# Kernel tuning notes

Hardware: AMD Instinct MI355X
Metric: run time of the kernel (lower is better)

## Reference

```python
import jax, jax.numpy as jnp
import numpy as np

H = 16
D_K = 64
WINDOW = 4  # hardcoded window_size in the original attention()


def setup_inputs() -> dict:
    key = jax.random.key(0)
    ks = jax.random.split(key, 11)
    B, S, D = 4, 2048, 1024
    s = 1.0 / np.sqrt(D)
    return {
        "query": jax.random.normal(ks[0], (B, S, D), jnp.float32),
        "key": jax.random.normal(ks[1], (B, S, D), jnp.float32),
        "value": jax.random.normal(ks[2], (B, S, D), jnp.float32),
        # torch Linear weights stored transposed ([in,out]) so y = x @ W + b
        "Wq": jax.random.normal(ks[3], (D, D), jnp.float32) * s,
        "bq": jnp.zeros((D,), jnp.float32),
        "Wk": jax.random.normal(ks[4], (D, D), jnp.float32) * s,
        "bk": jnp.zeros((D,), jnp.float32),
        "Wv": jax.random.normal(ks[5], (D, D), jnp.float32) * s,
        "bv": jnp.zeros((D,), jnp.float32),
        "Wo": jax.random.normal(ks[6], (D, D), jnp.float32) * s,
        "bo": jnp.zeros((D,), jnp.float32),
    }


def _split_heads(x, B, S):
    # [B,S,D] -> [B,H,S,d_k]
    return x.reshape(B, S, H, D_K).transpose(0, 2, 1, 3)


def reference(query, key, value, Wq, bq, Wk, bk, Wv, bv, Wo, bo):
    B, S, D = query.shape
    q = _split_heads(query @ Wq + bq, B, S)
    k = _split_heads(key @ Wk + bk, B, S)
    v = _split_heads(value @ Wv + bv, B, S)

    scores = jnp.einsum("bhqd,bhkd->bhqk", q, k) / np.sqrt(D_K)
    # banded local-window enhancement: double scores where |i-j| <= WINDOW
    i = jnp.arange(S)[:, None]
    j = jnp.arange(S)[None, :]
    band = (jnp.abs(i - j) <= WINDOW).astype(scores.dtype)  # [S,S]
    enhanced = scores * (1.0 + band)  # scores + scores*local_mask

    p_attn = jax.nn.softmax(enhanced, axis=-1)  # dropout = identity (eval)
    out = jnp.einsum("bhqk,bhkd->bhqd", p_attn, v)
    out = out.transpose(0, 2, 1, 3).reshape(B, S, D)
    return out @ Wo + bo
```

## Files before the change

### kernel.cpp

```cpp
#include <hip/hip_runtime.h>
#include <hip/hip_bf16.h>

typedef __attribute__((ext_vector_type(8))) short short8;
typedef __attribute__((ext_vector_type(4))) float f32x4;
typedef __attribute__((ext_vector_type(16))) float f32x16;

#define DEVINL static __device__ __forceinline__

DEVINL unsigned short f2b(float f) {
  __hip_bfloat16 h = __float2bfloat16(f);
  return __builtin_bit_cast(unsigned short, h);
}

DEVINL float fexp2(float x) {
#if __has_builtin(__builtin_amdgcn_exp2f)
  return __builtin_amdgcn_exp2f(x);
#else
  float r; asm("v_exp_f32 %0, %1\n\ts_nop 0" : "=v"(r) : "v"(x)); return r;
#endif
}

DEVINL unsigned cvt_pk_bf16(float a, float b) {
  unsigned r;
  asm("v_cvt_pk_bf16_f32 %0, %1, %2" : "=v"(r) : "v"(a), "v"(b));
  return r;
}

DEVINL void pl32swap(unsigned& a, unsigned& b) {
  asm volatile("v_permlane32_swap_b32 %0, %1" : "+v"(a), "+v"(b));
}

DEVINL void gload_lds16(const unsigned short* gsrc, unsigned short* ldst) {
  __builtin_amdgcn_global_load_lds(
      (const __attribute__((address_space(1))) unsigned int*)gsrc,
      (__attribute__((address_space(3))) unsigned int*)ldst,
      16, 0, 0);
}

__global__ __launch_bounds__(256)
void cvt_act_kernel(const float* __restrict__ in, unsigned short* __restrict__ out) {
  const long i = ((long)blockIdx.x * 256 + threadIdx.x) * 8;
  const float4 a = *reinterpret_cast<const float4*>(in + i);
  const float4 b = *reinterpret_cast<const float4*>(in + i + 4);
  uint4 o;
  o.x = f2b(a.x) | ((unsigned)f2b(a.y) << 16);
  o.y = f2b(a.z) | ((unsigned)f2b(a.w) << 16);
  o.z = f2b(b.x) | ((unsigned)f2b(b.y) << 16);
  o.w = f2b(b.z) | ((unsigned)f2b(b.w) << 16);
  *reinterpret_cast<uint4*>(out + i) = o;
}

__global__ __launch_bounds__(256)
void cvt_w_kernel(const float* __restrict__ W0, const float* __restrict__ W1,
                  const float* __restrict__ W2, const float* __restrict__ W3,
                  unsigned short* __restrict__ WtAll) {
  __shared__ __align__(16) unsigned short t[64][72];
  const float* W = blockIdx.z == 0 ? W0 : blockIdx.z == 1 ? W1 : blockIdx.z == 2 ? W2 : W3;
  unsigned short* out = WtAll + (size_t)blockIdx.z * (1024 * 1024);
  const int tid = threadIdx.x;
  const int k0 = blockIdx.y * 64, n0 = blockIdx.x * 64;
  const int r = tid >> 2;
  const int c = (tid & 3) * 16;
  #pragma unroll
  for (int u = 0; u < 4; ++u) {
    float4 v = *reinterpret_cast<const float4*>(W + (long)(k0 + r) * 1024 + n0 + c + u * 4);
    t[c + u*4 + 0][r] = f2b(v.x);
    t[c + u*4 + 1][r] = f2b(v.y);
    t[c + u*4 + 2][r] = f2b(v.z);
    t[c + u*4 + 3][r] = f2b(v.w);
  }
  __syncthreads();
  #pragma unroll
  for (int u = 0; u < 2; ++u)
    *reinterpret_cast<uint4*>(out + (long)(n0 + r) * 1024 + k0 + c + u * 8) =
        *reinterpret_cast<const uint4*>(&t[r][c + u * 8]);
}

template<int MODE>
__global__ __launch_bounds__(256)
void gemm_bf16_kernel(const unsigned short* __restrict__ A,
                      const unsigned short* __restrict__ Wt,
                      const float* __restrict__ bias, void* __restrict__ outp,
                      int M, int N, int K, float oscale)
{
  __shared__ __align__(16) unsigned short Asm[128 * 64];
  __shared__ __align__(16) unsigned short Bsm[128 * 64];

  const int tid = threadIdx.x;
  const int lane = tid & 63;
  const int wid = tid >> 6;
  const int l15 = lane & 15;
  const int lg  = lane >> 4;

  const int nwg = gridDim.x;
  const int cpx = nwg >> 3;
  const int wg  = blockIdx.x;
  const int swz = (wg & 7) * cpx + (wg >> 3);
  const int nbx = N >> 7;
  const long bm = (long)(swz / nbx) * 128;
  const long bn = (long)(swz % nbx) * 128;
  const int wm = (wid >> 1) * 64;
  const int wn = (wid & 1) * 64;

  const unsigned short* gA[4];
  const unsigned short* gB[4];
  unsigned ldsU[4];
  #pragma unroll
  for (int j = 0; j < 4; ++j) {
    const int t0 = j * 256 + wid * 64;
    const int task = t0 + lane;
    gA[j] = A  + (bm + (task >> 3)) * (long)K + (task & 7) * 8;
    gB[j] = Wt + (bn + (task >> 3)) * (long)K + (task & 7) * 8;
    ldsU[j] = (unsigned)t0 * 8;
  }

  f32x4 acc[4][4] = {};

  for (int kt = 0; kt < K; kt += 64) {
    #pragma unroll
    for (int j = 0; j < 4; ++j) {
      gload_lds16(gA[j] + kt, Asm + ldsU[j]);
      gload_lds16(gB[j] + kt, Bsm + ldsU[j]);
    }
    __syncthreads();

    short8 af[2][4], bf[2][4];
    #pragma unroll
    for (int m = 0; m < 4; ++m) {
      const unsigned short* pa = Asm + (wm + m * 16 + l15) * 64 + lg * 8;
      af[0][m] = *reinterpret_cast<const short8*>(pa);
      af[1][m] = *reinterpret_cast<const short8*>(pa + 32);
    }
    #pragma unroll
    for (int n = 0; n < 4; ++n) {
      const unsigned short* pb = Bsm + (wn + n * 16 + l15) * 64 + lg * 8;
      bf[0][n] = *reinterpret_cast<const short8*>(pb);
      bf[1][n] = *reinterpret_cast<const short8*>(pb + 32);
    }
    #pragma unroll
    for (int kk = 0; kk < 2; ++kk)
      #pragma unroll
      for (int m = 0; m < 4; ++m)
        #pragma unroll
        for (int n = 0; n < 4; ++n)
          acc[m][n] = __builtin_amdgcn_mfma_f32_16x16x32_bf16(af[kk][m], bf[kk][n], acc[m][n], 0, 0, 0);
    __syncthreads();
  }

  float bv[4];
  #pragma unroll
  for (int n = 0; n < 4; ++n) bv[n] = bias[bn + wn + n * 16 + l15];

  if (MODE == 1) {
    float* out = (float*)outp;
    #pragma unroll
    for (int m = 0; m < 4; ++m)
      #pragma unroll
      for (int r = 0; r < 4; ++r) {
        long row = bm + wm + m * 16 + lg * 4 + r;
        #pragma unroll
        for (int n = 0; n < 4; ++n)
          out[row * N + bn + wn + n * 16 + l15] = (acc[m][n][r] + bv[n]) * oscale;
      }
  } else if (MODE == 0) {
    unsigned short* out = (unsigned short*)outp;
    #pragma unroll
    for (int m = 0; m < 4; ++m)
      #pragma unroll
      for (int r = 0; r < 4; ++r) {
        long row = bm + wm + m * 16 + lg * 4 + r;
        long b = row >> 11, s = row & 2047;
        #pragma unroll
        for (int n = 0; n < 4; ++n) {
          long col = bn + wn + n * 16 + l15;
          long h = col >> 6, dk = col & 63;
          out[((((b << 4) + h) << 11) + s) * 64 + dk] = f2b((acc[m][n][r] + bv[n]) * oscale);
        }
      }
  } else {
    unsigned short* out = (unsigned short*)outp;
    #pragma unroll
    for (int m = 0; m < 4; ++m) {
      long row0 = bm + wm + m * 16 + lg * 4;
      long b = row0 >> 11, s0 = row0 & 2047;
      #pragma unroll
      for (int n = 0; n < 4; ++n) {
        long col = bn + wn + n * 16 + l15;
        long h = col >> 6, dk = col & 63;
        ushort4 hv;
        hv.x = f2b(acc[m][n][0] + bv[n]);
        hv.y = f2b(acc[m][n][1] + bv[n]);
        hv.z = f2b(acc[m][n][2] + bv[n]);
        hv.w = f2b(acc[m][n][3] + bv[n]);
        *reinterpret_cast<ushort4*>(&out[((((b << 4) + h) << 6) + dk) * 2048 + s0]) = hv;
      }
    }
  }
}

__global__ __launch_bounds__(512)
void attn_kernel(const unsigned short* __restrict__ Q,
                 const unsigned short* __restrict__ Kh,
                 const unsigned short* __restrict__ Vth,
                 unsigned short* __restrict__ Obf)
{
  __shared__ __align__(16) char lds[16384];

  const int tid = threadIdx.x;
  const int lane = tid & 63;
  const int w = tid >> 6;
  const int l31 = lane & 31;
  const int hi  = lane >> 5;
  const int r7  = l31 & 7;
  const int bh = blockIdx.x;
  const int wq = blockIdx.y * 256 + w * 32;
  const long base  = (long)bh * 2048 * 64;
  const long vbase = (long)bh * 64 * 2048;

  short8 aq[4];
  {
    const unsigned short* qp = Q + base + (long)(wq + l31) * 64 + hi * 8;
    #pragma unroll
    for (int sl = 0; sl < 4; ++sl)
      aq[sl] = *reinterpret_cast<const short8*>(qp + sl * 16);
  }

  const int srow = tid >> 3;
  const int sdst = (srow * 128 + (tid & 7) * 16) ^ ((srow & 7) << 4);
  const unsigned short* kgp = Kh + base + srow * 64 + (tid & 7) * 8;
  const unsigned short* vgp = Vth + vbase + (long)srow * 2048 + (tid & 7) * 8;

  uint4 kreg = *reinterpret_cast<const uint4*>(kgp);
  uint4 vreg = *reinterpret_cast<const uint4*>(vgp);

  f32x16 oacc0 = {}, oacc1 = {};
  float mrun = -1e30f, lrun = 0.f;

  for (int kvt = 0; kvt < 2048; kvt += 64) {
    __syncthreads();
    *reinterpret_cast<uint4*>(lds + sdst) = kreg;
    *reinterpret_cast<uint4*>(lds + 8192 + sdst) = vreg;
    __syncthreads();
    if (kvt + 64 < 2048) {
      kreg = *reinterpret_cast<const uint4*>(kgp + (kvt + 64) * 64);
      vreg = *reinterpret_cast<const uint4*>(vgp + (kvt + 64));
    }

    short8 ak[4][2], av[4][2];
    #pragma unroll
    for (int n = 0; n < 4; ++n) {
      #pragma unroll
      for (int half = 0; half < 2; ++half) {
        const int row = half * 32 + l31;
        const int slot = (((n * 2 + hi) ^ r7) << 4);
        ak[n][half] = *reinterpret_cast<const short8*>(lds + row * 128 + slot);
        av[n][half] = *reinterpret_cast<const short8*>(lds + 8192 + row * 128 + slot);
      }
    }

    f32x16 st0 = {}, st1 = {};
    #pragma unroll
    for (int sl = 0; sl < 4; ++sl) {
      st0 = __builtin_amdgcn_mfma_f32_32x32x16_bf16(ak[sl][0], aq[sl], st0, 0, 0, 0);
      st1 = __builtin_amdgcn_mfma_f32_32x32x16_bf16(ak[sl][1], aq[sl], st1, 0, 0, 0);
    }

    if ((kvt <= wq + 35) && (kvt + 67 >= wq)) {
      const int db0 = wq + l31 - kvt - 4 * hi;
      #pragma unroll
      for (int r = 0; r < 16; ++r) {
        const int rr = (r & 3) + 8 * (r >> 2);
        int d0 = db0 - rr;
        int d1 = db0 - 32 - rr;
        if (d0 >= -4 && d0 <= 4) st0[r] *= 2.f;
        if (d1 >= -4 && d1 <= 4) st1[r] *= 2.f;
      }
    }

    float tm[16];
    #pragma unroll
    for (int r = 0; r < 16; ++r) tm[r] = fmaxf(st0[r], st1[r]);
    #pragma unroll
    for (int s2 = 8; s2 >= 1; s2 >>= 1)
      #pragma unroll
      for (int r = 0; r < s2; ++r) tm[r] = fmaxf(tm[r], tm[r + s2]);
    float pmax = fmaxf(tm[0], __shfl_xor(tm[0], 32));

    if (pmax > mrun + 8.f) {
      float corr = fexp2(mrun - pmax);
      lrun *= corr;
      #pragma unroll
      for (int r = 0; r < 16; ++r) { oacc0[r] *= corr; oacc1[r] *= corr; }
      mrun = pmax;
    }

    #pragma unroll
    for (int r = 0; r < 16; ++r) {
      st0[r] = fexp2(st0[r] - mrun);
      st1[r] = fexp2(st1[r] - mrun);
    }
    float ts[16];
    #pragma unroll
    for (int r = 0; r < 16; ++r) ts[r] = st0[r] + st1[r];
    #pragma unroll
    for (int s2 = 8; s2 >= 1; s2 >>= 1)
      #pragma unroll
      for (int r = 0; r < s2; ++r) ts[r] += ts[r + s2];
    lrun += ts[0] + __shfl_xor(ts[0], 32);

    unsigned own0[8], own1[8];
    #pragma unroll
    for (int p = 0; p < 8; ++p) {
      own0[p] = cvt_pk_bf16(st0[2 * p], st0[2 * p + 1]);
      own1[p] = cvt_pk_bf16(st1[2 * p], st1[2 * p + 1]);
    }

    #pragma unroll
    for (int sl = 0; sl < 4; ++sl) {
      unsigned* ow = (sl < 2) ? own0 : own1;
      const int c4 = (sl & 1) * 4;
      pl32swap(ow[c4 + 0], ow[c4 + 2]);
      pl32swap(ow[c4 + 1], ow[c4 + 3]);
      uint4 pwv;
      pwv.x = ow[c4 + 0]; pwv.y = ow[c4 + 1]; pwv.z = ow[c4 + 2]; pwv.w = ow[c4 + 3];
      short8 pf = __builtin_bit_cast(short8, pwv);
      oacc0 = __builtin_amdgcn_mfma_f32_32x32x16_bf16(av[sl][0], pf, oacc0, 0, 0, 0);
      oacc1 = __builtin_amdgcn_mfma_f32_32x32x16_bf16(av[sl][1], pf, oacc1, 0, 0, 0);
    }
  }

  const int b = bh >> 4, h = bh & 15;
  const float inv = 1.f / lrun;
  unsigned short* op = Obf + ((long)(b * 2048 + wq + l31) << 10) + h * 64 + 4 * hi;
  #pragma unroll
  for (int g = 0; g < 4; ++g) {
    ushort4 u0, u1;
    u0.x = f2b(oacc0[4 * g + 0] * inv); u0.y = f2b(oacc0[4 * g + 1] * inv);
    u0.z = f2b(oacc0[4 * g + 2] * inv); u0.w = f2b(oacc0[4 * g + 3] * inv);
    u1.x = f2b(oacc1[4 * g + 0] * inv); u1.y = f2b(oacc1[4 * g + 1] * inv);
    u1.z = f2b(oacc1[4 * g + 2] * inv); u1.w = f2b(oacc1[4 * g + 3] * inv);
    *reinterpret_cast<ushort4*>(op + 8 * g) = u0;
    *reinterpret_cast<ushort4*>(op + 8 * g + 32) = u1;
  }
}

extern "C" void kernel_launch(void* const* d_in, const int* in_sizes, int n_in,
                              void* d_out, int out_size, void* d_ws, size_t ws_size,
                              hipStream_t stream)
{
  const float* query = (const float*)d_in[0];
  const float* key_  = (const float*)d_in[1];
  const float* value = (const float*)d_in[2];
  const float* Wq = (const float*)d_in[3];
  const float* bq = (const float*)d_in[4];
  const float* Wk = (const float*)d_in[5];
  const float* bk = (const float*)d_in[6];
  const float* Wv = (const float*)d_in[7];
  const float* bv = (const float*)d_in[8];
  const float* Wo = (const float*)d_in[9];
  const float* bo = (const float*)d_in[10];

  char* ws = (char*)d_ws;
  unsigned short* actbf = (unsigned short*)(ws);
  unsigned short* qh = (unsigned short*)(ws + ((size_t)16 << 20));
  unsigned short* kh = (unsigned short*)(ws + ((size_t)32 << 20));
  unsigned short* vt = (unsigned short*)(ws + ((size_t)48 << 20));
  unsigned short* WT = (unsigned short*)(ws + ((size_t)64 << 20));
  unsigned short* aout = actbf;

  const int Mrows = 4 * 2048, D = 1024;
  const float QSCALE = 0.125f * 1.44269504088896340736f;

  cvt_w_kernel<<<dim3(16, 16, 4), 256, 0, stream>>>(Wq, Wk, Wv, Wo, WT);

  cvt_act_kernel<<<4096, 256, 0, stream>>>(query, actbf);
  gemm_bf16_kernel<0><<<512, 256, 0, stream>>>(actbf, WT, bq, qh, Mrows, D, D, QSCALE);

  cvt_act_kernel<<<4096, 256, 0, stream>>>(key_, actbf);
  gemm_bf16_kernel<0><<<512, 256, 0, stream>>>(actbf, WT + (1 << 20), bk, kh, Mrows, D, D, 1.f);

  cvt_act_kernel<<<4096, 256, 0, stream>>>(value, actbf);
  gemm_bf16_kernel<2><<<512, 256, 0, stream>>>(actbf, WT + (2 << 20), bv, vt, Mrows, D, D, 1.f);

  attn_kernel<<<dim3(64, 8), 512, 0, stream>>>(qh, kh, vt, aout);

  gemm_bf16_kernel<1><<<512, 256, 0, stream>>>(aout, WT + (3 << 20), bo, (float*)d_out, Mrows, D, D, 1.f);
}
```

Baseline: 248.8 us.

## Fuse fp32-to-bf16 activation conversion into batched QKV projection GEMM

Removes the three separate activation conversion kernels. A single QKV GEMM launch with grid z=3 loads fp32 activations straight into registers, converts them to bf16 and stores them into LDS, with the next tile's A loads issued during the MFMA compute. This avoids writing and rereading a bf16 copy of each activation and cuts the number of launches. The trade-off is that A is now staged through registers instead of the direct global-to-LDS path, and fp32 reads each K tile twice as many bytes, which may lower GEMM efficiency.

New measurement: 224.9 us. -9.6%, faster.

```diff
diff --git a/kernel.cpp b/kernel.cpp
--- a/kernel.cpp
+++ b/kernel.cpp
@@ -35,19 +35,6 @@
       (const __attribute__((address_space(1))) unsigned int*)gsrc,
       (__attribute__((address_space(3))) unsigned int*)ldst,
       16, 0, 0);
-}
-
-__global__ __launch_bounds__(256)
-void cvt_act_kernel(const float* __restrict__ in, unsigned short* __restrict__ out) {
-  const long i = ((long)blockIdx.x * 256 + threadIdx.x) * 8;
-  const float4 a = *reinterpret_cast<const float4*>(in + i);
-  const float4 b = *reinterpret_cast<const float4*>(in + i + 4);
-  uint4 o;
-  o.x = f2b(a.x) | ((unsigned)f2b(a.y) << 16);
-  o.y = f2b(a.z) | ((unsigned)f2b(a.w) << 16);
-  o.z = f2b(b.x) | ((unsigned)f2b(b.y) << 16);
-  o.w = f2b(b.z) | ((unsigned)f2b(b.w) << 16);
-  *reinterpret_cast<uint4*>(out + i) = o;
 }
 
 __global__ __launch_bounds__(256)
@@ -76,15 +63,24 @@
         *reinterpret_cast<const uint4*>(&t[r][c + u * 8]);
 }
 
-template<int MODE>
 __global__ __launch_bounds__(256)
-void gemm_bf16_kernel(const unsigned short* __restrict__ A,
-                      const unsigned short* __restrict__ Wt,
-                      const float* __restrict__ bias, void* __restrict__ outp,
-                      int M, int N, int K, float oscale)
+void qkv_gemm_kernel(const float* __restrict__ Aq, const float* __restrict__ Ak,
+                     const float* __restrict__ Av,
+                     const unsigned short* __restrict__ WTall,
+                     const float* __restrict__ bq, const float* __restrict__ bk,
+                     const float* __restrict__ bv,
+                     unsigned short* __restrict__ qh, unsigned short* __restrict__ kh,
+                     unsigned short* __restrict__ vt, float qscale)
 {
+  constexpr int N = 1024, K = 1024;
   __shared__ __align__(16) unsigned short Asm[128 * 64];
   __shared__ __align__(16) unsigned short Bsm[128 * 64];
+
+  const int z = blockIdx.z;
+  const float* A = z == 0 ? Aq : z == 1 ? Ak : Av;
+  const unsigned short* Wt = WTall + ((size_t)z << 20);
+  const float* bias = z == 0 ? bq : z == 1 ? bk : bv;
+  const float oscale = z == 0 ? qscale : 1.f;
 
   const int tid = threadIdx.x;
   const int lane = tid & 63;
@@ -102,27 +98,50 @@
   const int wm = (wid >> 1) * 64;
   const int wn = (wid & 1) * 64;
 
-  const unsigned short* gA[4];
+  const float* gAf[4];
   const unsigned short* gB[4];
   unsigned ldsU[4];
+  int ldsE[4];
   #pragma unroll
   for (int j = 0; j < 4; ++j) {
     const int t0 = j * 256 + wid * 64;
     const int task = t0 + lane;
-    gA[j] = A  + (bm + (task >> 3)) * (long)K + (task & 7) * 8;
-    gB[j] = Wt + (bn + (task >> 3)) * (long)K + (task & 7) * 8;
+    gAf[j] = A  + (bm + (task >> 3)) * (long)K + (task & 7) * 8;
+    gB[j]  = Wt + (bn + (task >> 3)) * (long)K + (task & 7) * 8;
     ldsU[j] = (unsigned)t0 * 8;
+    ldsE[j] = task * 8;
   }
 
   f32x4 acc[4][4] = {};
 
+  float4 ra[4][2];
+  #pragma unroll
+  for (int j = 0; j < 4; ++j) {
+    ra[j][0] = *reinterpret_cast<const float4*>(gAf[j]);
+    ra[j][1] = *reinterpret_cast<const float4*>(gAf[j] + 4);
+  }
+
   for (int kt = 0; kt < K; kt += 64) {
     #pragma unroll
+    for (int j = 0; j < 4; ++j)
+      gload_lds16(gB[j] + kt, Bsm + ldsU[j]);
+    #pragma unroll
     for (int j = 0; j < 4; ++j) {
-      gload_lds16(gA[j] + kt, Asm + ldsU[j]);
-      gload_lds16(gB[j] + kt, Bsm + ldsU[j]);
-    }
-    __syncthreads();
+      uint4 o;
+      o.x = cvt_pk_bf16(ra[j][0].x, ra[j][0].y);
+      o.y = cvt_pk_bf16(ra[j][0].z, ra[j][0].w);
+      o.z = cvt_pk_bf16(ra[j][1].x, ra[j][1].y);
+      o.w = cvt_pk_bf16(ra[j][1].z, ra[j][1].w);
+      *reinterpret_cast<uint4*>(Asm + ldsE[j]) = o;
+    }
+    __syncthreads();
+    if (kt + 64 < K) {
+      #pragma unroll
+      for (int j = 0; j < 4; ++j) {
+        ra[j][0] = *reinterpret_cast<const float4*>(gAf[j] + kt + 64);
+        ra[j][1] = *reinterpret_cast<const float4*>(gAf[j] + kt + 68);
+      }
+    }
 
     short8 af[2][4], bf[2][4];
     #pragma unroll
@@ -147,23 +166,12 @@
     __syncthreads();
   }
 
-  float bv[4];
-  #pragma unroll
-  for (int n = 0; n < 4; ++n) bv[n] = bias[bn + wn + n * 16 + l15];
-
-  if (MODE == 1) {
-    float* out = (float*)outp;
-    #pragma unroll
-    for (int m = 0; m < 4; ++m)
-      #pragma unroll
-      for (int r = 0; r < 4; ++r) {
-        long row = bm + wm + m * 16 + lg * 4 + r;
-        #pragma unroll
-        for (int n = 0; n < 4; ++n)
-          out[row * N + bn + wn + n * 16 + l15] = (acc[m][n][r] + bv[n]) * oscale;
-      }
-  } else if (MODE == 0) {
-    unsigned short* out = (unsigned short*)outp;
+  float bvv[4];
+  #pragma unroll
+  for (int n = 0; n < 4; ++n) bvv[n] = bias[bn + wn + n * 16 + l15];
+
+  if (z < 2) {
+    unsigned short* out = z == 0 ? qh : kh;
     #pragma unroll
     for (int m = 0; m < 4; ++m)
       #pragma unroll
@@ -174,11 +182,11 @@
         for (int n = 0; n < 4; ++n) {
           long col = bn + wn + n * 16 + l15;
           long h = col >> 6, dk = col & 63;
-          out[((((b << 4) + h) << 11) + s) * 64 + dk] = f2b((acc[m][n][r] + bv[n]) * oscale);
+          out[((((b << 4) + h) << 11) + s) * 64 + dk] = f2b((acc[m][n][r] + bvv[n]) * oscale);
         }
       }
   } else {
-    unsigned short* out = (unsigned short*)outp;
+    unsigned short* out = vt;
     #pragma unroll
     for (int m = 0; m < 4; ++m) {
       long row0 = bm + wm + m * 16 + lg * 4;
@@ -188,14 +196,99 @@
         long col = bn + wn + n * 16 + l15;
         long h = col >> 6, dk = col & 63;
         ushort4 hv;
-        hv.x = f2b(acc[m][n][0] + bv[n]);
-        hv.y = f2b(acc[m][n][1] + bv[n]);
-        hv.z = f2b(acc[m][n][2] + bv[n]);
-        hv.w = f2b(acc[m][n][3] + bv[n]);
+        hv.x = f2b(acc[m][n][0] + bvv[n]);
+        hv.y = f2b(acc[m][n][1] + bvv[n]);
+        hv.z = f2b(acc[m][n][2] + bvv[n]);
+        hv.w = f2b(acc[m][n][3] + bvv[n]);
         *reinterpret_cast<ushort4*>(&out[((((b << 4) + h) << 6) + dk) * 2048 + s0]) = hv;
       }
     }
   }
+}
+
+__global__ __launch_bounds__(256)
+void gemm_out_kernel(const unsigned short* __restrict__ A,
+                     const unsigned short* __restrict__ Wt,
+                     const float* __restrict__ bias, float* __restrict__ out,
+                     int M, int N, int K)
+{
+  __shared__ __align__(16) unsigned short Asm[128 * 64];
+  __shared__ __align__(16) unsigned short Bsm[128 * 64];
+
+  const int tid = threadIdx.x;
+  const int lane = tid & 63;
+  const int wid = tid >> 6;
+  const int l15 = lane & 15;
+  const int lg  = lane >> 4;
+
+  const int nwg = gridDim.x;
+  const int cpx = nwg >> 3;
+  const int wg  = blockIdx.x;
+  const int swz = (wg & 7) * cpx + (wg >> 3);
+  const int nbx = N >> 7;
+  const long bm = (long)(swz / nbx) * 128;
+  const long bn = (long)(swz % nbx) * 128;
+  const int wm = (wid >> 1) * 64;
+  const int wn = (wid & 1) * 64;
+
+  const unsigned short* gA[4];
+  const unsigned short* gB[4];
+  unsigned ldsU[4];
+  #pragma unroll
+  for (int j = 0; j < 4; ++j) {
+    const int t0 = j * 256 + wid * 64;
+    const int task = t0 + lane;
+    gA[j] = A  + (bm + (task >> 3)) * (long)K + (task & 7) * 8;
+    gB[j] = Wt + (bn + (task >> 3)) * (long)K + (task & 7) * 8;
+    ldsU[j] = (unsigned)t0 * 8;
+  }
+
+  f32x4 acc[4][4] = {};
+
+  for (int kt = 0; kt < K; kt += 64) {
+    #pragma unroll
+    for (int j = 0; j < 4; ++j) {
+      gload_lds16(gA[j] + kt, Asm + ldsU[j]);
+      gload_lds16(gB[j] + kt, Bsm + ldsU[j]);
+    }
+    __syncthreads();
+
+    short8 af[2][4], bf[2][4];
+    #pragma unroll
+    for (int m = 0; m < 4; ++m) {
+      const unsigned short* pa = Asm + (wm + m * 16 + l15) * 64 + lg * 8;
+      af[0][m] = *reinterpret_cast<const short8*>(pa);
+      af[1][m] = *reinterpret_cast<const short8*>(pa + 32);
+    }
+    #pragma unroll
+    for (int n = 0; n < 4; ++n) {
+      const unsigned short* pb = Bsm + (wn + n * 16 + l15) * 64 + lg * 8;
+      bf[0][n] = *reinterpret_cast<const short8*>(pb);
+      bf[1][n] = *reinterpret_cast<const short8*>(pb + 32);
+    }
+    #pragma unroll
+    for (int kk = 0; kk < 2; ++kk)
+      #pragma unroll
+      for (int m = 0; m < 4; ++m)
+        #pragma unroll
+        for (int n = 0; n < 4; ++n)
+          acc[m][n] = __builtin_amdgcn_mfma_f32_16x16x32_bf16(af[kk][m], bf[kk][n], acc[m][n], 0, 0, 0);
+    __syncthreads();
+  }
+
+  float bvv[4];
+  #pragma unroll
+  for (int n = 0; n < 4; ++n) bvv[n] = bias[bn + wn + n * 16 + l15];
+
+  #pragma unroll
+  for (int m = 0; m < 4; ++m)
+    #pragma unroll
+    for (int r = 0; r < 4; ++r) {
+      long row = bm + wm + m * 16 + lg * 4 + r;
+      #pragma unroll
+      for (int n = 0; n < 4; ++n)
+        out[row * N + bn + wn + n * 16 + l15] = acc[m][n][r] + bvv[n];
+    }
 }
 
 __global__ __launch_bounds__(512)
@@ -361,28 +454,22 @@
   const float* bo = (const float*)d_in[10];
 
   char* ws = (char*)d_ws;
-  unsigned short* actbf = (unsigned short*)(ws);
+  unsigned short* aout = (unsigned short*)(ws);
   unsigned short* qh = (unsigned short*)(ws + ((size_t)16 << 20));
   unsigned short* kh = (unsigned short*)(ws + ((size_t)32 << 20));
   unsigned short* vt = (unsigned short*)(ws + ((size_t)48 << 20));
   unsigned short* WT = (unsigned short*)(ws + ((size_t)64 << 20));
-  unsigned short* aout = actbf;
 
   const int Mrows = 4 * 2048, D = 1024;
   const float QSCALE = 0.125f * 1.44269504088896340736f;
 
   cvt_w_kernel<<<dim3(16, 16, 4), 256, 0, stream>>>(Wq, Wk, Wv, Wo, WT);
 
-  cvt_act_kernel<<<4096, 256, 0, stream>>>(query, actbf);
-  gemm_bf16_kernel<0><<<512, 256, 0, stream>>>(actbf, WT, bq, qh, Mrows, D, D, QSCALE);
-
-  cvt_act_kernel<<<4096, 256, 0, stream>>>(key_, actbf);
-  gemm_bf16_kernel<0><<<512, 256, 0, stream>>>(actbf, WT + (1 << 20), bk, kh, Mrows, D, D, 1.f);
-
-  cvt_act_kernel<<<4096, 256, 0, stream>>>(value, actbf);
-  gemm_bf16_kernel<2><<<512, 256, 0, stream>>>(actbf, WT + (2 << 20), bv, vt, Mrows, D, D, 1.f);
+  qkv_gemm_kernel<<<dim3(512, 1, 3), 256, 0, stream>>>(
+      query, key_, value, WT, bq, bk, bv, qh, kh, vt, QSCALE);
 
   attn_kernel<<<dim3(64, 8), 512, 0, stream>>>(qh, kh, vt, aout);
 
-  gemm_bf16_kernel<1><<<512, 256, 0, stream>>>(aout, WT + (3 << 20), bo, (float*)d_out, Mrows, D, D, 1.f);
-}
+  gemm_out_kernel<<<512, 256, 0, stream>>>(aout, WT + (3 << 20), bo,
+                                           (float*)d_out, Mrows, D, D);
+}
```
